# Optimization experiments

Hardware: AMD Instinct MI355X
Metric: run time of the kernel (lower is better)

Reference implementation:

```python
import jax, jax.numpy as jnp
import numpy as np
import math

NUM_HEADS = 16
HEAD_SIZE = 64
SEQ_LEN = 2048
D_MODEL = NUM_HEADS * HEAD_SIZE
BATCH = 2


def _xavier(key, shape):
    fan_in, fan_out = shape[0], shape[1]
    limit = math.sqrt(6.0 / (fan_in + fan_out))
    return jax.random.uniform(key, shape, jnp.float32, -limit, limit)


def setup_inputs() -> dict:
    key = jax.random.key(0)
    ks = jax.random.split(key, 5)
    x = jax.random.normal(ks[0], (BATCH, SEQ_LEN, D_MODEL), jnp.float32)
    W_Q = _xavier(ks[1], (D_MODEL, D_MODEL))
    W_K = _xavier(ks[2], (D_MODEL, D_MODEL))
    W_V = _xavier(ks[3], (D_MODEL, D_MODEL))
    W_O = _xavier(ks[4], (D_MODEL, D_MODEL))
    zeros = jnp.zeros((D_MODEL,), jnp.float32)
    return {
        "x": x,
        "W_Q": W_Q, "W_K": W_K, "W_V": W_V, "W_O": W_O,
        "b_Q": zeros, "b_K": zeros, "b_V": zeros, "b_O": zeros,
    }


def _split_heads(t):
    # [B, S, H*d] -> [B, H, S, d]
    B, S, _ = t.shape
    return t.reshape(B, S, NUM_HEADS, HEAD_SIZE).transpose(0, 2, 1, 3)


def reference(x, W_Q, W_K, W_V, W_O, b_Q, b_K, b_V, b_O):
    q = _split_heads(x @ W_Q + b_Q)  # [B,H,S,d]
    k = _split_heads(x @ W_K + b_K)
    v = _split_heads(x @ W_V + b_V)

    # scores: [B,H,S,S]
    scores = jnp.einsum("bhqd,bhkd->bhqk", q, k)
    # Faithful to original: multiply by lower-triangular 0/1 mask, scale,
    # then add -10000 on strictly-upper positions (NOT -inf).
    tril = jnp.tril(jnp.ones((SEQ_LEN, SEQ_LEN), jnp.float32))
    neg_bias = jnp.triu(jnp.full((SEQ_LEN, SEQ_LEN), -10000.0, jnp.float32), 1)
    masked = scores * tril / np.sqrt(HEAD_SIZE).astype(np.float32) + neg_bias
    weights = jax.nn.softmax(masked, axis=-1)

    hs = jnp.einsum("bhqk,bhkd->bhqd", weights, v)  # [B,H,S,d]
    B = hs.shape[0]
    merged = hs.transpose(0, 2, 1, 3).reshape(B, SEQ_LEN, D_MODEL)
    return merged @ W_O + b_O
```

## Files before the change

kernel.cpp:

```cpp
#include <hip/hip_runtime.h>
#include <hip/hip_bf16.h>

#define S_LEN 2048
#define NH 16
#define HD 64
#define DM 1024
#define BATCH 2
#define M_ROWS (BATCH * S_LEN)
#define SCALE2 0.18033688011112043f
#define M2FIX 8.0f

typedef float f32x4 __attribute__((ext_vector_type(4)));
typedef float f32x16 __attribute__((ext_vector_type(16)));
typedef __bf16 bf16x8 __attribute__((ext_vector_type(8)));
typedef short short8 __attribute__((ext_vector_type(8)));

__device__ __forceinline__ unsigned short f2bf(float f) {
  unsigned u = __builtin_bit_cast(unsigned, f);
  u += 0x7FFFu + ((u >> 16) & 1u);
  return (unsigned short)(u >> 16);
}

__device__ __forceinline__ f32x4 mfma16(bf16x8 a, bf16x8 b, f32x4 c) {
  return __builtin_amdgcn_mfma_f32_16x16x32_bf16(a, b, c, 0, 0, 0);
}

__device__ __forceinline__ f32x16 mfma32(bf16x8 a, bf16x8 b, f32x16 c) {
  return __builtin_amdgcn_mfma_f32_32x32x16_bf16(a, b, c, 0, 0, 0);
}

__device__ __forceinline__ void gload_lds16(const void* g, void* l) {
  __builtin_amdgcn_global_load_lds(
      (const __attribute__((address_space(1))) void*)g,
      (__attribute__((address_space(3))) void*)l, 16, 0, 0);
}

__global__ __launch_bounds__(256) void cast_bf16_kernel(
    const float* __restrict__ in, unsigned short* __restrict__ out) {
  int i = blockIdx.x * 256 + threadIdx.x;
  const float4* p = (const float4*)in;
  float4 f0 = p[i * 2], f1 = p[i * 2 + 1];
  short8 o;
  o[0] = (short)f2bf(f0.x); o[1] = (short)f2bf(f0.y);
  o[2] = (short)f2bf(f0.z); o[3] = (short)f2bf(f0.w);
  o[4] = (short)f2bf(f1.x); o[5] = (short)f2bf(f1.y);
  o[6] = (short)f2bf(f1.z); o[7] = (short)f2bf(f1.w);
  ((short8*)out)[i] = o;
}

__global__ __launch_bounds__(256) void transpose_cast_kernel(
    const float* __restrict__ W0, const float* __restrict__ W1,
    const float* __restrict__ W2, const float* __restrict__ W3,
    unsigned short* __restrict__ out) {
  int z = blockIdx.z;
  const float* W = (z == 0) ? W0 : (z == 1) ? W1 : (z == 2) ? W2 : W3;
  __shared__ float tile[32][33];
  int tx = threadIdx.x & 31, ty = threadIdx.x >> 5;
  int bx = blockIdx.x * 32, by = blockIdx.y * 32;
#pragma unroll
  for (int i = 0; i < 4; ++i)
    tile[ty + i * 8][tx] = W[(size_t)(by + ty + i * 8) * DM + bx + tx];
  __syncthreads();
  unsigned short* o = out + (size_t)z * DM * DM;
#pragma unroll
  for (int i = 0; i < 4; ++i)
    o[(size_t)(bx + ty + i * 8) * DM + by + tx] = f2bf(tile[tx][ty + i * 8]);
}

__global__ __launch_bounds__(512, 2) void gemm_qkv256_kernel(
    const unsigned short* __restrict__ A, const unsigned short* __restrict__ Bt,
    unsigned short* __restrict__ Cb, const float* __restrict__ bQ,
    const float* __restrict__ bK, const float* __restrict__ bV) {
  const int t = threadIdx.x, lane = t & 63;
  const int wid = t >> 6, wr = wid >> 2, wc = wid & 3;
  const int r16 = lane & 15, g = lane >> 4;
  const int K = 1024, nk = 32;

  const int lid = blockIdx.x;
  const int xcd = lid & 7, idx = lid >> 3;
  const int by = xcd * 2 + (idx >= 12);
  const int bx = (idx >= 12) ? idx - 12 : idx;
  const int m0 = by * 256, n0 = bx * 256;

  __shared__ __align__(16) char LB[98304];

  const int c0 = t, c1 = t + 512;
  const int pr0 = c0 >> 3, v0 = (c0 & 7) ^ (pr0 & 7);
  const int pr1 = c1 >> 3, v1 = (c1 & 7) ^ (pr1 & 7);
  const int ar0 = 2 * pr0 + (v0 >> 2), ak0 = (v0 & 3) * 8;
  const int ar1 = 2 * pr1 + (v1 >> 2), ak1 = (v1 & 3) * 8;

#define ASLOT(s) ((unsigned short*)(LB + (s) * 16384))
#define BSLOT(s) ((unsigned short*)(LB + 49152 + (s) * 16384))
#define STAGE_A(s, k0)                                                        \
  gload_lds16(A + (size_t)(m0 + ar0) * K + (k0) + ak0, ASLOT(s) + c0 * 8);    \
  gload_lds16(A + (size_t)(m0 + ar1) * K + (k0) + ak1, ASLOT(s) + c1 * 8);
#define STAGE_B(s, k0)                                                        \
  gload_lds16(Bt + (size_t)(n0 + ar0) * K + (k0) + ak0, BSLOT(s) + c0 * 8);   \
  gload_lds16(Bt + (size_t)(n0 + ar1) * K + (k0) + ak1, BSLOT(s) + c1 * 8);

  const int S16 = ((r16 & 1) * 4 + g) ^ (r16 >> 1);
  const int aoff = (r16 >> 1) * 128 + S16 * 16;

  f32x4 acc[8][4] = {};

  STAGE_A(0, 0); STAGE_B(0, 0);
  STAGE_A(1, 32); STAGE_B(1, 32);
  asm volatile("s_waitcnt vmcnt(4)" ::: "memory");
  __builtin_amdgcn_s_barrier();

  for (int j = 0; j < nk; ++j) {
    const int cs = j % 3, ps = (j + 2) % 3;
    const char* As_ = (const char*)ASLOT(cs);
    const char* Bs_ = (const char*)BSLOT(cs);

    bf16x8 af[4], bf[4];
#pragma unroll
    for (int mi = 0; mi < 4; ++mi)
      af[mi] = *(const bf16x8*)(As_ + (wr * 64 + mi * 8) * 128 + aoff);
#pragma unroll
    for (int ni = 0; ni < 4; ++ni)
      bf[ni] = *(const bf16x8*)(Bs_ + (wc * 32 + ni * 8) * 128 + aoff);
    if (j + 2 < nk) { STAGE_A(ps, (j + 2) * 32); }
    __builtin_amdgcn_s_barrier();
    asm volatile("s_waitcnt lgkmcnt(0)" ::: "memory");
    __builtin_amdgcn_s_setprio(1);
#pragma unroll
    for (int mi = 0; mi < 4; ++mi)
#pragma unroll
      for (int ni = 0; ni < 4; ++ni)
        acc[mi][ni] = mfma16(af[mi], bf[ni], acc[mi][ni]);
    __builtin_amdgcn_s_setprio(0);
    __builtin_amdgcn_s_barrier();

    bf16x8 af2[4];
#pragma unroll
    for (int mi = 0; mi < 4; ++mi)
      af2[mi] = *(const bf16x8*)(As_ + (wr * 64 + 32 + mi * 8) * 128 + aoff);
    if (j + 2 < nk) { STAGE_B(ps, (j + 2) * 32); }
    __builtin_amdgcn_s_barrier();
    asm volatile("s_waitcnt lgkmcnt(0)" ::: "memory");
    __builtin_amdgcn_s_setprio(1);
#pragma unroll
    for (int mi = 0; mi < 4; ++mi)
#pragma unroll
      for (int ni = 0; ni < 4; ++ni)
        acc[4 + mi][ni] = mfma16(af2[mi], bf[ni], acc[4 + mi][ni]);
    __builtin_amdgcn_s_setprio(0);

    if (j + 1 < nk) {
      if (j + 2 < nk) {
        asm volatile("s_waitcnt vmcnt(4)" ::: "memory");
      } else {
        asm volatile("s_waitcnt vmcnt(0)" ::: "memory");
      }
    }
    __builtin_amdgcn_s_barrier();
  }
#undef STAGE_A
#undef STAGE_B

  const int bufq = n0 >> 10;
  if (bufq < 2) {
    const float* bp = bufq ? bK : bQ;
    const float sc = bufq ? 1.0f : SCALE2;
#pragma unroll
    for (int ni = 0; ni < 4; ++ni) {
      int cn = (n0 & 1023) + wc * 64 + ni * 16 + r16;
      float bv = bp[cn];
#pragma unroll
      for (int mi = 0; mi < 8; ++mi) {
        int row = m0 + wr * 128 + mi * 16 + 4 * g;
#pragma unroll
        for (int jj = 0; jj < 4; ++jj)
          Cb[(size_t)bufq * 4194304u + (size_t)(row + jj) * 1024 + cn] =
              __builtin_bit_cast(unsigned short, (__bf16)((acc[mi][ni][jj] + bv) * sc));
      }
    }
  } else {
    unsigned short* T = (unsigned short*)LB;
    const int bb = m0 >> 11, s0g = m0 & 2047;
    unsigned short* Vt = Cb + 8388608u;
#pragma unroll
    for (int ph = 0; ph < 2; ++ph) {
      __syncthreads();
      if ((wc >> 1) == ph) {
#pragma unroll
        for (int ni = 0; ni < 4; ++ni) {
          int cnl = (wc & 1) * 64 + ni * 16 + r16;
          float bv = bV[(n0 & 1023) + ph * 128 + cnl];
#pragma unroll
          for (int mi = 0; mi < 8; ++mi) {
            int sl = wr * 128 + mi * 16 + 4 * g;
            union { __bf16 h4[4]; uint2 u; } cv;
#pragma unroll
            for (int jj = 0; jj < 4; ++jj) cv.h4[jj] = (__bf16)(acc[mi][ni][jj] + bv);
            *(uint2*)&T[cnl * 264 + sl] = cv.u;
          }
        }
      }
      __syncthreads();
#pragma unroll
      for (int q = 0; q < 8; ++q) {
        int idx2 = q * 512 + t;
        int cnl = idx2 >> 5, sch = idx2 & 31;
        int cng = (n0 & 1023) + ph * 128 + cnl;
        int hh = cng >> 6, d = cng & 63;
        short8 v = *(const short8*)&T[cnl * 264 + sch * 8];
        *(short8*)&Vt[(((size_t)((bb * 16 + hh) * 64 + d)) << 11) + s0g + sch * 8] = v;
      }
    }
  }
}

__global__ __launch_bounds__(256) void gemm_out_kernel(
    const unsigned short* __restrict__ A, const unsigned short* __restrict__ Bt,
    float* __restrict__ Cf, const float* __restrict__ bias0, int M, int N, int K) {
  __shared__ __align__(16) unsigned short As[3][4096];
  __shared__ __align__(16) unsigned short Bs[3][4096];
  const int t = threadIdx.x, lane = t & 63;
  const int wid = t >> 6, wr = wid >> 1, wc = wid & 1;
  const int r16 = lane & 15, g = lane >> 4;
  const int m0 = blockIdx.y * 128, n0 = blockIdx.x * 128;
  const int nk = K >> 5;

  const int n1 = t, n2 = t + 256;
  const int r1g = t >> 2;
  const int r2g = r1g + 64;
  const int c1g = ((t & 3) ^ (r1g & 3)) * 8;

  const unsigned short* ap1 = A + (size_t)(m0 + r1g) * K + c1g;
  const unsigned short* ap2 = A + (size_t)(m0 + r2g) * K + c1g;
  const unsigned short* bp1 = Bt + (size_t)(n0 + r1g) * K + c1g;
  const unsigned short* bp2 = Bt + (size_t)(n0 + r2g) * K + c1g;

#define GSTAGE(s)                          \
  gload_lds16(ap1, &As[s][n1 * 8]);        \
  gload_lds16(bp1, &Bs[s][n1 * 8]);        \
  gload_lds16(ap2, &As[s][n2 * 8]);        \
  gload_lds16(bp2, &Bs[s][n2 * 8]);        \
  ap1 += 32; ap2 += 32; bp1 += 32; bp2 += 32;

  f32x4 acc[4][4] = {};
  GSTAGE(0);
  GSTAGE(1);

  const int axr = ((g ^ (r16 & 3)) * 8);

  for (int kt = 0; kt < nk; ++kt) {
    const int cs = kt % 3;
    if (kt + 1 < nk) {
      asm volatile("s_waitcnt vmcnt(4)" ::: "memory");
    } else {
      asm volatile("s_waitcnt vmcnt(0)" ::: "memory");
    }
    __builtin_amdgcn_s_barrier();
    if (kt + 2 < nk) { GSTAGE((kt + 2) % 3); }

    bf16x8 af[4], bfr[4];
#pragma unroll
    for (int mi = 0; mi < 4; ++mi)
      af[mi] = *(const bf16x8*)&As[cs][(wr * 64 + mi * 16 + r16) * 32 + axr];
#pragma unroll
    for (int ni = 0; ni < 4; ++ni)
      bfr[ni] = *(const bf16x8*)&Bs[cs][(wc * 64 + ni * 16 + r16) * 32 + axr];
    __builtin_amdgcn_s_setprio(1);
#pragma unroll
    for (int mi = 0; mi < 4; ++mi)
#pragma unroll
      for (int ni = 0; ni < 4; ++ni)
        acc[mi][ni] = mfma16(af[mi], bfr[ni], acc[mi][ni]);
    __builtin_amdgcn_s_setprio(0);
  }
#undef GSTAGE

#pragma unroll
  for (int ni = 0; ni < 4; ++ni) {
    int col = n0 + wc * 64 + ni * 16 + r16;
    float bv = bias0[col];
#pragma unroll
    for (int mi = 0; mi < 4; ++mi) {
      int rowb = m0 + wr * 64 + mi * 16 + 4 * g;
#pragma unroll
      for (int j = 0; j < 4; ++j)
        Cf[(size_t)(rowb + j) * N + col] = acc[mi][ni][j] + bv;
    }
  }
}

__global__ __launch_bounds__(256, 2) void attn_kernel(
    const unsigned short* __restrict__ Qm, const unsigned short* __restrict__ Km,
    const unsigned short* __restrict__ VtG, unsigned short* __restrict__ Om) {
  const int t = threadIdx.x, lane = t & 63, w = t >> 6;
  const int l31 = lane & 31, hi = lane >> 5;
  const int bid = blockIdx.x;
  const int xk = bid & 7, slot = bid >> 3;
  const int grp = xk * 4 + (slot >> 4);
  const int mq = slot & 15;
  const int h = grp & 15, b = grp >> 4;

  __shared__ __align__(16) char LB[71680];
  float* R = (float*)LB;
  float* ls = (float*)(LB + 69632);

  const unsigned short* Kbase = Km + (size_t)(b * S_LEN) * DM + h * HD;
  const unsigned short* Vbase = VtG + (size_t)((b * NH + h) * HD) * S_LEN;

  const int kg = ((t & 7) ^ ((t >> 3) & 7)) * 8;
  const int kr0 = t >> 3;
  const int vg = ((t & 15) ^ ((t >> 4) & 15)) * 8;
  const int vr0 = t >> 4;

  auto stage = [&](int cs, int kv0) {
    unsigned short* kd = (unsigned short*)(LB + cs * 16384) + t * 8;
    unsigned short* vd = (unsigned short*)(LB + 32768 + cs * 16384) + t * 8;
#pragma unroll
    for (int p = 0; p < 4; ++p)
      gload_lds16(Kbase + (size_t)(kv0 + kr0 + 32 * p) * DM + kg, kd + 2048 * p);
#pragma unroll
    for (int p = 0; p < 4; ++p)
      gload_lds16(Vbase + (size_t)(vr0 + 16 * p) * S_LEN + kv0 + vg, vd + 2048 * p);
  };

  for (int half = 0; half < 2; ++half) {
    const int T = half ? 31 - mq : mq;
    const int q0 = T * 64;

    bf16x8 qfr[2][4];
#pragma unroll
    for (int qt = 0; qt < 2; ++qt) {
      const unsigned short* Qp =
          Qm + (size_t)(b * S_LEN + q0 + qt * 32 + l31) * DM + h * HD;
#pragma unroll
      for (int kc = 0; kc < 4; ++kc)
        qfr[qt][kc] = *(const bf16x8*)(Qp + kc * 16 + hi * 8);
    }

    f32x16 oacc[2][2] = {};
    float lsum0 = 0.f, lsum1 = 0.f;
    const int ntk = (T >> 1) + 1;

    stage(0, 0);

    for (int kt = 0; kt < ntk; ++kt) {
      const int cs = kt & 1;
      asm volatile("s_waitcnt vmcnt(0)" ::: "memory");
      __builtin_amdgcn_s_barrier();
      if (kt + 1 < ntk) stage(cs ^ 1, (kt + 1) * 128);

      const int kv0w = kt * 128 + w * 32;
      if (kv0w <= q0 + 63) {
        const unsigned short* Ksb = (const unsigned short*)(LB + cs * 16384);
        const unsigned short* Vsb = (const unsigned short*)(LB + 32768 + cs * 16384);

        bf16x8 kf[4];
#pragma unroll
        for (int kc = 0; kc < 4; ++kc)
          kf[kc] = *(const bf16x8*)&Ksb[(w * 32 + l31) * 64 +
                                        (((hi + 2 * kc) ^ (lane & 7)) * 8)];
        bool act0 = false, act1 = false;
        bf16x8 pfr[2][2];
#pragma unroll
        for (int qt = 0; qt < 2; ++qt) {
          const bool act = (kv0w <= q0 + qt * 32 + 31);
          if (qt == 0) act0 = act; else act1 = act;
          if (!act) continue;
          f32x16 st = {};
          __builtin_amdgcn_s_setprio(1);
#pragma unroll
          for (int kc = 0; kc < 4; ++kc) st = mfma32(kf[kc], qfr[qt][kc], st);
          __builtin_amdgcn_s_setprio(0);

          const bool needmask = (kv0w + 31 > q0 + qt * 32);
          const int qg = q0 + qt * 32 + l31;
          float p[16];
          float ps = 0.f;
#pragma unroll
          for (int r = 0; r < 16; ++r) {
            int row = (r & 3) + 8 * (r >> 2) + 4 * hi;
            float v = __builtin_amdgcn_exp2f(st[r] - M2FIX);
            if (needmask && (kv0w + row > qg)) v = 0.f;
            p[r] = v;
            ps += v;
          }
          if (qt == 0) lsum0 += ps; else lsum1 += ps;

          unsigned pw[8];
#pragma unroll
          for (int r = 0; r < 8; ++r) {
            union { __bf16 h2[2]; unsigned u; } cv;
            cv.h2[0] = (__bf16)p[2 * r];
            cv.h2[1] = (__bf16)p[2 * r + 1];
            pw[r] = cv.u;
          }
          {
            auto s0 = __builtin_amdgcn_permlane32_swap(pw[0], pw[2], false, false);
            pw[0] = s0[0]; pw[2] = s0[1];
            auto s1 = __builtin_amdgcn_permlane32_swap(pw[1], pw[3], false, false);
            pw[1] = s1[0]; pw[3] = s1[1];
            auto s2 = __builtin_amdgcn_permlane32_swap(pw[4], pw[6], false, false);
            pw[4] = s2[0]; pw[6] = s2[1];
            auto s3 = __builtin_amdgcn_permlane32_swap(pw[5], pw[7], false, false);
            pw[5] = s3[0]; pw[7] = s3[1];
          }
          union { unsigned u[4]; bf16x8 v; } f0, f1;
          f0.u[0] = pw[0]; f0.u[1] = pw[1]; f0.u[2] = pw[2]; f0.u[3] = pw[3];
          f1.u[0] = pw[4]; f1.u[1] = pw[5]; f1.u[2] = pw[6]; f1.u[3] = pw[7];
          pfr[qt][0] = f0.v;
          pfr[qt][1] = f1.v;
        }

        bf16x8 vf[2][2];
#pragma unroll
        for (int dt = 0; dt < 2; ++dt)
#pragma unroll
          for (int ks = 0; ks < 2; ++ks)
            vf[dt][ks] = *(const bf16x8*)&Vsb[(dt * 32 + l31) * 128 +
                                              (((4 * w + 2 * ks + hi) ^ (lane & 15)) * 8)];
        __builtin_amdgcn_s_setprio(1);
        if (act0) {
#pragma unroll
          for (int dt = 0; dt < 2; ++dt) {
            oacc[dt][0] = mfma32(vf[dt][0], pfr[0][0], oacc[dt][0]);
            oacc[dt][0] = mfma32(vf[dt][1], pfr[0][1], oacc[dt][0]);
          }
        }
        if (act1) {
#pragma unroll
          for (int dt = 0; dt < 2; ++dt) {
            oacc[dt][1] = mfma32(vf[dt][0], pfr[1][0], oacc[dt][1]);
            oacc[dt][1] = mfma32(vf[dt][1], pfr[1][1], oacc[dt][1]);
          }
        }
        __builtin_amdgcn_s_setprio(0);
      }
    }

    __syncthreads();
    float* Rw = R + w * 4352;
#pragma unroll
    for (int dt = 0; dt < 2; ++dt)
#pragma unroll
      for (int qt = 0; qt < 2; ++qt) {
        int q = qt * 32 + l31;
#pragma unroll
        for (int r = 0; r < 16; r += 2) {
          int d = dt * 32 + ((r & 3) + 8 * (r >> 2)) + 4 * hi;
          float2 v2;
          v2.x = oacc[dt][qt][r];
          v2.y = oacc[dt][qt][r + 1];
          *(float2*)&Rw[q * 68 + d] = v2;
        }
      }
    ls[(w * 64 + l31) * 2 + hi] = lsum0;
    ls[(w * 64 + 32 + l31) * 2 + hi] = lsum1;
    __syncthreads();

    const int rq = t >> 2, dq = (t & 3) * 16;
    f32x4 a0 = {}, a1 = {}, a2 = {}, a3 = {};
#pragma unroll
    for (int w4 = 0; w4 < 4; ++w4) {
      const float* Rb = R + w4 * 4352 + rq * 68 + dq;
      a0 += *(const f32x4*)&Rb[0];
      a1 += *(const f32x4*)&Rb[4];
      a2 += *(const f32x4*)&Rb[8];
      a3 += *(const f32x4*)&Rb[12];
    }
    float s = 0.f;
#pragma unroll
    for (int w4 = 0; w4 < 4; ++w4)
      s += ls[(w4 * 64 + rq) * 2] + ls[(w4 * 64 + rq) * 2 + 1];
    float li = 1.0f / s;
    unsigned short* op = Om + (size_t)(b * S_LEN + q0 + rq) * DM + h * HD + dq;
    union { __bf16 hh[8]; uint4 u; } o0, o1;
#pragma unroll
    for (int i = 0; i < 4; ++i) {
      o0.hh[i] = (__bf16)(a0[i] * li);
      o0.hh[4 + i] = (__bf16)(a1[i] * li);
      o1.hh[i] = (__bf16)(a2[i] * li);
      o1.hh[4 + i] = (__bf16)(a3[i] * li);
    }
    *(uint4*)op = o0.u;
    *(uint4*)(op + 8) = o1.u;
    __syncthreads();
  }
}

extern "C" void kernel_launch(void* const* d_in, const int* in_sizes, int n_in,
                              void* d_out, int out_size, void* d_ws, size_t ws_size,
                              hipStream_t stream) {
  (void)in_sizes; (void)n_in; (void)out_size; (void)ws_size;
  const float* x  = (const float*)d_in[0];
  const float* WQ = (const float*)d_in[1];
  const float* WK = (const float*)d_in[2];
  const float* WV = (const float*)d_in[3];
  const float* WO = (const float*)d_in[4];
  const float* bQ = (const float*)d_in[5];
  const float* bK = (const float*)d_in[6];
  const float* bV = (const float*)d_in[7];
  const float* bO = (const float*)d_in[8];

  char* ws = (char*)d_ws;
  unsigned short* xb  = (unsigned short*)(ws);
  unsigned short* wt  = (unsigned short*)(ws + (8u << 20));
  unsigned short* qb  = (unsigned short*)(ws + (16u << 20));
  unsigned short* hsb = (unsigned short*)(ws + (40u << 20));

  cast_bf16_kernel<<<2048, 256, 0, stream>>>(x, xb);
  transpose_cast_kernel<<<dim3(32, 32, 4), 256, 0, stream>>>(WQ, WK, WV, WO, wt);
  gemm_qkv256_kernel<<<192, 512, 0, stream>>>(xb, wt, qb, bQ, bK, bV);
  attn_kernel<<<512, 256, 0, stream>>>(qb, qb + 4194304u, qb + 8388608u, hsb);
  gemm_out_kernel<<<dim3(8, 32), 256, 0, stream>>>(
      hsb, wt + 3u * 1048576u, (float*)d_out, bO, M_ROWS, DM, DM);
}
```

Baseline: 110.3 us.

## Rework QKV GEMM to BK=64 double-buffered ping-pong schedule; drop out-GEMM LDS swizzle

Restructures the QKV projection GEMM main loop to use K-tiles of 64 with double buffering (128KB LDS) instead of 32-wide triple buffering. Each iteration runs four MFMA phases over quadrant sub-tiles, interleaved with staged loads. A new XOR swizzle is applied to the LDS layout. The output GEMM's LDS swizzle is also removed in favor of plain row-major addressing, which may introduce bank conflicts. The goal is to halve the loop iterations and barrier overhead per K, at the cost of more LDS use and a different conflict pattern.

```diff
diff --git a/kernel.cpp b/kernel.cpp
--- a/kernel.cpp
+++ b/kernel.cpp
@@ -74,7 +74,7 @@
   const int t = threadIdx.x, lane = t & 63;
   const int wid = t >> 6, wr = wid >> 2, wc = wid & 3;
   const int r16 = lane & 15, g = lane >> 4;
-  const int K = 1024, nk = 32;
+  const int K = 1024, nt = 16;
 
   const int lid = blockIdx.x;
   const int xcd = lid & 7, idx = lid >> 3;
@@ -82,83 +82,132 @@
   const int bx = (idx >= 12) ? idx - 12 : idx;
   const int m0 = by * 256, n0 = bx * 256;
 
-  __shared__ __align__(16) char LB[98304];
-
-  const int c0 = t, c1 = t + 512;
-  const int pr0 = c0 >> 3, v0 = (c0 & 7) ^ (pr0 & 7);
-  const int pr1 = c1 >> 3, v1 = (c1 & 7) ^ (pr1 & 7);
-  const int ar0 = 2 * pr0 + (v0 >> 2), ak0 = (v0 & 3) * 8;
-  const int ar1 = 2 * pr1 + (v1 >> 2), ak1 = (v1 & 3) * 8;
-
-#define ASLOT(s) ((unsigned short*)(LB + (s) * 16384))
-#define BSLOT(s) ((unsigned short*)(LB + 49152 + (s) * 16384))
-#define STAGE_A(s, k0)                                                        \
-  gload_lds16(A + (size_t)(m0 + ar0) * K + (k0) + ak0, ASLOT(s) + c0 * 8);    \
-  gload_lds16(A + (size_t)(m0 + ar1) * K + (k0) + ak1, ASLOT(s) + c1 * 8);
-#define STAGE_B(s, k0)                                                        \
-  gload_lds16(Bt + (size_t)(n0 + ar0) * K + (k0) + ak0, BSLOT(s) + c0 * 8);   \
-  gload_lds16(Bt + (size_t)(n0 + ar1) * K + (k0) + ak1, BSLOT(s) + c1 * 8);
-
-  const int S16 = ((r16 & 1) * 4 + g) ^ (r16 >> 1);
-  const int aoff = (r16 >> 1) * 128 + S16 * 16;
+  __shared__ __align__(16) char LB[131072];
+
+  const int r0 = t >> 3;
+  const int gk = ((t & 7) ^ (((t >> 5) & 1) << 1)) * 8;
+
+  auto stageA = [&](int s, int kt) {
+#pragma unroll
+    for (int h = 0; h < 2; ++h) {
+      char* dst = LB + (s * 2 + h) * 16384 + t * 16;
+      const unsigned short* src = A + (size_t)(m0 + h * 128 + r0) * K + kt * 64 + gk;
+      gload_lds16(src, dst);
+      gload_lds16(src + (size_t)64 * K, dst + 8192);
+    }
+  };
+  auto stageB = [&](int s, int kt) {
+#pragma unroll
+    for (int h = 0; h < 2; ++h) {
+      char* dst = LB + 65536 + (s * 2 + h) * 16384 + t * 16;
+      const unsigned short* src = Bt + (size_t)(n0 + h * 128 + r0) * K + kt * 64 + gk;
+      gload_lds16(src, dst);
+      gload_lds16(src + (size_t)64 * K, dst + 8192);
+    }
+  };
+
+  const int aoff = (r16 * 128 + g * 16) ^ ((r16 & 4) << 3);
 
   f32x4 acc[8][4] = {};
 
-  STAGE_A(0, 0); STAGE_B(0, 0);
-  STAGE_A(1, 32); STAGE_B(1, 32);
+  stageA(0, 0);
+  stageB(0, 0);
+  stageA(1, 1);
   asm volatile("s_waitcnt vmcnt(4)" ::: "memory");
   __builtin_amdgcn_s_barrier();
 
-  for (int j = 0; j < nk; ++j) {
-    const int cs = j % 3, ps = (j + 2) % 3;
-    const char* As_ = (const char*)ASLOT(cs);
-    const char* Bs_ = (const char*)BSLOT(cs);
-
-    bf16x8 af[4], bf[4];
-#pragma unroll
-    for (int mi = 0; mi < 4; ++mi)
-      af[mi] = *(const bf16x8*)(As_ + (wr * 64 + mi * 8) * 128 + aoff);
-#pragma unroll
-    for (int ni = 0; ni < 4; ++ni)
-      bf[ni] = *(const bf16x8*)(Bs_ + (wc * 32 + ni * 8) * 128 + aoff);
-    if (j + 2 < nk) { STAGE_A(ps, (j + 2) * 32); }
+#pragma unroll 1
+  for (int j = 0; j < 16; ++j) {
+    const int p = j & 1;
+    const char* Ah = LB + (p * 2 + wr) * 16384;
+    const char* Bh = LB + 65536 + (p * 2 + (wc >> 1)) * 16384 + (wc & 1) * 8192;
+
+    bf16x8 afr[4][2], bfr[2][2], b2[2][2];
+
+#pragma unroll
+    for (int mi = 0; mi < 4; ++mi)
+#pragma unroll
+      for (int ks = 0; ks < 2; ++ks)
+        afr[mi][ks] = *(const bf16x8*)(Ah + mi * 2048 + ks * 64 + aoff);
+#pragma unroll
+    for (int ni = 0; ni < 2; ++ni)
+#pragma unroll
+      for (int ks = 0; ks < 2; ++ks)
+        bfr[ni][ks] = *(const bf16x8*)(Bh + ni * 2048 + ks * 64 + aoff);
+    if (j + 1 < nt) stageB(p ^ 1, j + 1);
     __builtin_amdgcn_s_barrier();
     asm volatile("s_waitcnt lgkmcnt(0)" ::: "memory");
     __builtin_amdgcn_s_setprio(1);
 #pragma unroll
     for (int mi = 0; mi < 4; ++mi)
 #pragma unroll
-      for (int ni = 0; ni < 4; ++ni)
-        acc[mi][ni] = mfma16(af[mi], bf[ni], acc[mi][ni]);
+      for (int ni = 0; ni < 2; ++ni)
+#pragma unroll
+        for (int ks = 0; ks < 2; ++ks)
+          acc[mi][ni] = mfma16(afr[mi][ks], bfr[ni][ks], acc[mi][ni]);
     __builtin_amdgcn_s_setprio(0);
     __builtin_amdgcn_s_barrier();
 
-    bf16x8 af2[4];
-#pragma unroll
-    for (int mi = 0; mi < 4; ++mi)
-      af2[mi] = *(const bf16x8*)(As_ + (wr * 64 + 32 + mi * 8) * 128 + aoff);
-    if (j + 2 < nk) { STAGE_B(ps, (j + 2) * 32); }
+#pragma unroll
+    for (int ni = 0; ni < 2; ++ni)
+#pragma unroll
+      for (int ks = 0; ks < 2; ++ks)
+        b2[ni][ks] = *(const bf16x8*)(Bh + 4096 + ni * 2048 + ks * 64 + aoff);
     __builtin_amdgcn_s_barrier();
     asm volatile("s_waitcnt lgkmcnt(0)" ::: "memory");
     __builtin_amdgcn_s_setprio(1);
 #pragma unroll
     for (int mi = 0; mi < 4; ++mi)
 #pragma unroll
-      for (int ni = 0; ni < 4; ++ni)
-        acc[4 + mi][ni] = mfma16(af2[mi], bf[ni], acc[4 + mi][ni]);
+      for (int ni = 0; ni < 2; ++ni)
+#pragma unroll
+        for (int ks = 0; ks < 2; ++ks)
+          acc[mi][2 + ni] = mfma16(afr[mi][ks], b2[ni][ks], acc[mi][2 + ni]);
     __builtin_amdgcn_s_setprio(0);
-
-    if (j + 1 < nk) {
-      if (j + 2 < nk) {
-        asm volatile("s_waitcnt vmcnt(4)" ::: "memory");
-      } else {
-        asm volatile("s_waitcnt vmcnt(0)" ::: "memory");
-      }
+    __builtin_amdgcn_s_barrier();
+
+#pragma unroll
+    for (int mi = 0; mi < 4; ++mi)
+#pragma unroll
+      for (int ks = 0; ks < 2; ++ks)
+        afr[mi][ks] = *(const bf16x8*)(Ah + 8192 + mi * 2048 + ks * 64 + aoff);
+    __builtin_amdgcn_s_barrier();
+    asm volatile("s_waitcnt lgkmcnt(0)" ::: "memory");
+    __builtin_amdgcn_s_setprio(1);
+#pragma unroll
+    for (int mi = 0; mi < 4; ++mi)
+#pragma unroll
+      for (int ni = 0; ni < 2; ++ni)
+#pragma unroll
+        for (int ks = 0; ks < 2; ++ks)
+          acc[4 + mi][2 + ni] = mfma16(afr[mi][ks], b2[ni][ks], acc[4 + mi][2 + ni]);
+    __builtin_amdgcn_s_setprio(0);
+    __builtin_amdgcn_s_barrier();
+
+#pragma unroll
+    for (int ni = 0; ni < 2; ++ni)
+#pragma unroll
+      for (int ks = 0; ks < 2; ++ks)
+        bfr[ni][ks] = *(const bf16x8*)(Bh + ni * 2048 + ks * 64 + aoff);
+    if (j + 2 < nt) stageA(p, j + 2);
+    __builtin_amdgcn_s_barrier();
+    asm volatile("s_waitcnt lgkmcnt(0)" ::: "memory");
+    __builtin_amdgcn_s_setprio(1);
+#pragma unroll
+    for (int mi = 0; mi < 4; ++mi)
+#pragma unroll
+      for (int ni = 0; ni < 2; ++ni)
+#pragma unroll
+        for (int ks = 0; ks < 2; ++ks)
+          acc[4 + mi][ni] = mfma16(afr[mi][ks], bfr[ni][ks], acc[4 + mi][ni]);
+    __builtin_amdgcn_s_setprio(0);
+    if (j + 2 < nt) {
+      asm volatile("s_waitcnt vmcnt(4)" ::: "memory");
+    } else {
+      asm volatile("s_waitcnt vmcnt(0)" ::: "memory");
     }
     __builtin_amdgcn_s_barrier();
   }
-#undef STAGE_A
-#undef STAGE_B
 
   const int bufq = n0 >> 10;
   if (bufq < 2) {
@@ -225,9 +274,8 @@
   const int nk = K >> 5;
 
   const int n1 = t, n2 = t + 256;
-  const int r1g = t >> 2;
-  const int r2g = r1g + 64;
-  const int c1g = ((t & 3) ^ (r1g & 3)) * 8;
+  const int r1g = t >> 2, c1g = (t & 3) * 8;
+  const int r2g = (t + 256) >> 2;
 
   const unsigned short* ap1 = A + (size_t)(m0 + r1g) * K + c1g;
   const unsigned short* ap2 = A + (size_t)(m0 + r2g) * K + c1g;
@@ -245,8 +293,6 @@
   GSTAGE(0);
   GSTAGE(1);
 
-  const int axr = ((g ^ (r16 & 3)) * 8);
-
   for (int kt = 0; kt < nk; ++kt) {
     const int cs = kt % 3;
     if (kt + 1 < nk) {
@@ -260,10 +306,10 @@
     bf16x8 af[4], bfr[4];
 #pragma unroll
     for (int mi = 0; mi < 4; ++mi)
-      af[mi] = *(const bf16x8*)&As[cs][(wr * 64 + mi * 16 + r16) * 32 + axr];
+      af[mi] = *(const bf16x8*)&As[cs][(wr * 64 + mi * 16 + r16) * 32 + g * 8];
 #pragma unroll
     for (int ni = 0; ni < 4; ++ni)
-      bfr[ni] = *(const bf16x8*)&Bs[cs][(wc * 64 + ni * 16 + r16) * 32 + axr];
+      bfr[ni] = *(const bf16x8*)&Bs[cs][(wc * 64 + ni * 16 + r16) * 32 + g * 8];
     __builtin_amdgcn_s_setprio(1);
 #pragma unroll
     for (int mi = 0; mi < 4; ++mi)
```

After: 114.0 us. +3.3%, slower.
